# Performance work log

Hardware: AMD Instinct MI355X
Metric: run time of the kernel (lower is better)

The kernel has to match this reference:

```python
import jax, jax.numpy as jnp
import numpy as np

B, T, I, H, O = 64, 512, 128, 1024, 128
ALPHA = 0.2


def setup_inputs() -> dict:
    key = jax.random.key(0)
    ks = jax.random.split(key, 7)
    inv_sqrt_h = 1.0 / np.sqrt(H)
    return {
        "x": jax.random.normal(ks[0], (B, T, I), dtype=jnp.float32),
        "wi": jax.random.normal(ks[1], (I, H), dtype=jnp.float32) / np.sqrt(I),
        "wrec": jax.random.normal(ks[2], (H, H), dtype=jnp.float32) * inv_sqrt_h,
        "wout": jax.random.normal(ks[3], (H, O), dtype=jnp.float32) * inv_sqrt_h,
        "b": jax.random.normal(ks[4], (H, 1), dtype=jnp.float32) * 0.1,
        "g": jax.random.normal(ks[5], (H, 1), dtype=jnp.float32) * 0.5 + 1.0,
        "h0": jax.random.normal(ks[6], (H,), dtype=jnp.float32) * 0.1,
    }


def reference(x, wi, wrec, wout, b, g, h0):
    # Leaky tanh RNN: h_{t+1} = h_t + alpha*(-h_t + (g*r_t) @ wrec^T + x_t @ wi)
    #                 r_t = tanh(h_t + b); out_t = (g*r_t) @ wout
    gv = g[:, 0]  # (H,)
    bv = b[:, 0]  # (H,)
    batch = x.shape[0]

    r0 = jnp.tanh(h0 + bv)                     # (H,)
    out0 = (gv * r0) @ wout                    # (O,) broadcast over batch

    h_init = jnp.broadcast_to(h0, (batch, h0.shape[0]))
    r_init = jnp.broadcast_to(r0, (batch, h0.shape[0]))

    # precompute input projection for all steps used in the loop (steps 0..T-2)
    xs = jnp.swapaxes(x[:, :-1, :], 0, 1)      # (T-1, B, I)

    def step(carry, x_t):
        h, r = carry
        h = h + ALPHA * (-h + (gv * r) @ wrec.T + x_t @ wi)
        r = jnp.tanh(h + bv)
        out = (gv * r) @ wout                  # (B, O)
        return (h, r), out

    _, outs = jax.lax.scan(step, (h_init, r_init), xs)   # (T-1, B, O)
    outs = jnp.swapaxes(outs, 0, 1)                      # (B, T-1, O)
    out0b = jnp.broadcast_to(out0, (batch, 1, wout.shape[1]))
    return jnp.concatenate([out0b, outs], axis=1)        # (B, T, O)
```

## Files before the change

### kernel.cpp

```cpp
#include <hip/hip_runtime.h>

#define H 1024
#define I_DIM 128
#define O_DIM 128
#define T_DIM 512
#define ALPHA 0.2f
#define NWG 64
#define GSZ 16

typedef short short8 __attribute__((ext_vector_type(8)));
typedef float f32x4 __attribute__((ext_vector_type(4)));
typedef unsigned long long ull_alias __attribute__((may_alias));

__device__ __forceinline__ unsigned short f2b(float f) {
    union { float f; unsigned u; } x; x.f = f;
    unsigned u = x.u;
    return (unsigned short)((u + 0x7FFFu + ((u >> 16) & 1u)) >> 16);
}
__device__ __forceinline__ float tanh_fast(float x) {
    float e = __expf(2.0f * x);
    return 1.0f - 2.0f * __builtin_amdgcn_rcpf(e + 1.0f);
}
__device__ __forceinline__ short8 ld8f(const float* __restrict__ p) {
    const float4 a = *(const float4*)p;
    const float4 b = *(const float4*)(p + 4);
    short8 r;
    r[0]=(short)f2b(a.x); r[1]=(short)f2b(a.y); r[2]=(short)f2b(a.z); r[3]=(short)f2b(a.w);
    r[4]=(short)f2b(b.x); r[5]=(short)f2b(b.y); r[6]=(short)f2b(b.z); r[7]=(short)f2b(b.w);
    return r;
}

__global__ __launch_bounds__(256, 1) void rnn_kernel(
    const float* __restrict__ x, const float* __restrict__ wi,
    const float* __restrict__ wrec, const float* __restrict__ wout,
    const float* __restrict__ bb, const float* __restrict__ gg,
    const float* __restrict__ h0p, float* __restrict__ out,
    unsigned short* __restrict__ aG, unsigned int* __restrict__ tagG)
{
    __shared__ unsigned short abuf[32 * 512];
    __shared__ unsigned short aloc[1024];
    __shared__ float opart[4 * 128];

    const int tid  = threadIdx.x;
    const int w    = tid >> 6, lane = tid & 63;
    const int n    = lane & 15, q = lane >> 4;
    const int grp  = blockIdx.x & 3;
    const int ji   = blockIdx.x >> 2;
    const int j0   = ji * 64;
    const int j    = j0 + w * 16 + n;
    const int b0   = grp * 16;
    unsigned int* tg = tagG + grp * 128;

    short8 wfr[32];
#pragma unroll
    for (int kt = 0; kt < 32; ++kt)
        wfr[kt] = ld8f(&wrec[(size_t)j * H + kt * 32 + q * 8]);

    short8 wifr[4];
#pragma unroll
    for (int kt = 0; kt < 4; ++kt) {
        short8 v;
#pragma unroll
        for (int i = 0; i < 8; ++i)
            v[i] = (short)f2b(wi[(size_t)(kt * 32 + q * 8 + i) * H + j]);
        wifr[kt] = v;
    }
    short8 wofr[8];
#pragma unroll
    for (int kk = 0; kk < 8; ++kk) {
        short8 v;
        const int kb = (w * 8 + kk) * 32 + q * 8;
#pragma unroll
        for (int i = 0; i < 8; ++i)
            v[i] = (n < 8) ? (short)f2b(wout[(size_t)(kb + i) * O_DIM + ji * 8 + n]) : (short)0;
        wofr[kk] = v;
    }

    const float gv = gg[j], bv = bb[j], h00 = h0p[j];
    float hreg[4];
#pragma unroll
    for (int r = 0; r < 4; ++r) hreg[r] = h00;

    const int kl    = w * 16 + n;
    const int off_l = (kl >> 5) * 512 + ((kl & 31) >> 3) * 128 + (kl & 7);
    const int slot  = ji * 4 + w;

    auto publish = [&](int t) {
        asm volatile("" ::: "memory");
        unsigned long long v = *(const ull_alias*)&aloc[w * 256 + lane * 4];
        unsigned long long* dst = (unsigned long long*)
            (aG + (size_t)((t & 1) * 4 + grp) * 16384 + ji * 1024 + w * 256 + lane * 4);
        __hip_atomic_store(dst, v, __ATOMIC_RELAXED, __HIP_MEMORY_SCOPE_AGENT);
        asm volatile("s_waitcnt vmcnt(0)" ::: "memory");
        if (lane == 0)
            __hip_atomic_store(&tg[(t & 1) * 64 + slot], (unsigned)t,
                               __ATOMIC_RELAXED, __HIP_MEMORY_SCOPE_AGENT);
    };

    auto consume = [&](int tv) {
        const ull_alias* s64 = (const ull_alias*)
            (aG + (size_t)((tv & 1) * 4 + grp) * 16384) + (size_t)w * 1024;
        unsigned long long vals[16];
#pragma unroll
        for (int i = 0; i < 16; ++i)
            vals[i] = __hip_atomic_load((const unsigned long long*)&s64[i * 64 + lane],
                                        __ATOMIC_RELAXED, __HIP_MEMORY_SCOPE_AGENT);
        asm volatile("" ::: "memory");
        ull_alias* d64 = (ull_alias*)abuf + (size_t)w * 1024;
#pragma unroll
        for (int i = 0; i < 16; ++i)
            d64[i * 64 + lane] = vals[i];
    };

    auto do_out = [&](int t) {
        f32x4 oa = {0.f, 0.f, 0.f, 0.f};
#pragma unroll
        for (int kk = 0; kk < 8; ++kk) {
            short8 af = *(const short8*)&abuf[(w * 8 + kk) * 512 + lane * 8];
            oa = __builtin_amdgcn_mfma_f32_16x16x32_bf16(af, wofr[kk], oa, 0, 0, 0);
        }
        if (n < 8) {
#pragma unroll
            for (int r = 0; r < 4; ++r) opart[w * 128 + (4 * q + r) * 8 + n] = oa[r];
        }
        __syncthreads();
        if (tid < 128) {
            float s = opart[tid] + opart[128 + tid] + opart[256 + tid] + opart[384 + tid];
            const int m = tid >> 3, c = tid & 7;
            out[((size_t)(b0 + m) * T_DIM + t) * O_DIM + ji * 8 + c] = s;
        }
    };

    auto wait_tags = [&](int tv) {
        const unsigned int* tp = tg + (tv & 1) * 64;
        for (;;) {
            unsigned v = __hip_atomic_load(&tp[lane], __ATOMIC_RELAXED,
                                           __HIP_MEMORY_SCOPE_AGENT);
            if (__all(v == (unsigned)tv)) break;
            __builtin_amdgcn_s_sleep(1);
        }
        asm volatile("" ::: "memory");
    };

    {
        unsigned short a0 = f2b(gv * tanh_fast(h00 + bv));
#pragma unroll
        for (int r = 0; r < 4; ++r) aloc[off_l + (4 * q + r) * 8] = a0;
        publish(0);
    }

    short8 xfr[4];
#pragma unroll
    for (int kt = 0; kt < 4; ++kt)
        xfr[kt] = ld8f(&x[(size_t)(b0 + n) * T_DIM * I_DIM + kt * 32 + q * 8]);

    for (int t = 1; t < T_DIM; ++t) {
        f32x4 acc0 = {0.f,0.f,0.f,0.f}, acc1 = {0.f,0.f,0.f,0.f};
        acc0 = __builtin_amdgcn_mfma_f32_16x16x32_bf16(xfr[0], wifr[0], acc0, 0,0,0);
        acc1 = __builtin_amdgcn_mfma_f32_16x16x32_bf16(xfr[1], wifr[1], acc1, 0,0,0);
        acc0 = __builtin_amdgcn_mfma_f32_16x16x32_bf16(xfr[2], wifr[2], acc0, 0,0,0);
        acc1 = __builtin_amdgcn_mfma_f32_16x16x32_bf16(xfr[3], wifr[3], acc1, 0,0,0);

        __syncthreads();
        wait_tags(t - 1);
        consume(t - 1);
        __syncthreads();

#pragma unroll
        for (int kt = 0; kt < 32; kt += 2) {
            short8 a0f = *(const short8*)&abuf[kt * 512 + lane * 8];
            short8 a1f = *(const short8*)&abuf[(kt + 1) * 512 + lane * 8];
            acc0 = __builtin_amdgcn_mfma_f32_16x16x32_bf16(a0f, wfr[kt],     acc0, 0,0,0);
            acc1 = __builtin_amdgcn_mfma_f32_16x16x32_bf16(a1f, wfr[kt + 1], acc1, 0,0,0);
        }

#pragma unroll
        for (int r = 0; r < 4; ++r) {
            float z  = acc0[r] + acc1[r];
            float hv = (1.0f - ALPHA) * hreg[r] + ALPHA * z;
            hreg[r] = hv;
            aloc[off_l + (4 * q + r) * 8] = f2b(gv * tanh_fast(hv + bv));
        }
        publish(t);

        if (t < T_DIM - 1) {
#pragma unroll
            for (int kt = 0; kt < 4; ++kt)
                xfr[kt] = ld8f(&x[((size_t)(b0 + n) * T_DIM + t) * I_DIM + kt * 32 + q * 8]);
        }
        do_out(t - 1);
    }

    __syncthreads();
    wait_tags(T_DIM - 1);
    consume(T_DIM - 1);
    __syncthreads();
    do_out(T_DIM - 1);
}

extern "C" void kernel_launch(void* const* d_in, const int* in_sizes, int n_in,
                              void* d_out, int out_size, void* d_ws, size_t ws_size,
                              hipStream_t stream) {
    const float* x    = (const float*)d_in[0];
    const float* wi   = (const float*)d_in[1];
    const float* wrec = (const float*)d_in[2];
    const float* wout = (const float*)d_in[3];
    const float* bb   = (const float*)d_in[4];
    const float* gg   = (const float*)d_in[5];
    const float* h0   = (const float*)d_in[6];
    float* outp = (float*)d_out;

    unsigned short* aG = (unsigned short*)d_ws;
    unsigned int* tagG = (unsigned int*)((char*)d_ws + 2 * 4 * 16384 * 2);

    hipMemsetAsync(tagG, 0xFF, 4 * 2 * 64 * sizeof(unsigned int), stream);
    hipLaunchKernelGGL(rnn_kernel, dim3(NWG), dim3(256), 0, stream,
                       x, wi, wrec, wout, bb, gg, h0, outp, aG, tagG);
}
```

Before: 1.961 ms.

## Embed step tags in published activation words to drop separate flag handshake

Each 64-bit published word now carries 48 bits of bf16 activation data plus a 16-bit step tag, so consumers poll the data itself instead of waiting on a separate tag array. This removes the vmcnt wait and separate tag store on the producer side and the extra tag-polling round trip on the consumer side, shortening the per-step cross-workgroup latency. The cost is extra pack/unpack bit manipulation and about 1.5x more global traffic per step. Correctness depends on 64-bit atomic stores being seen whole, and the tag repeats only after 65536 steps.

```diff
diff --git a/kernel.cpp b/kernel.cpp
--- a/kernel.cpp
+++ b/kernel.cpp
@@ -7,6 +7,8 @@
 #define ALPHA 0.2f
 #define NWG 64
 #define GSZ 16
+#define SLICE_U64 96
+#define GRP_U64   (64 * SLICE_U64)
 
 typedef short short8 __attribute__((ext_vector_type(8)));
 typedef float f32x4 __attribute__((ext_vector_type(4)));
@@ -35,7 +37,7 @@
     const float* __restrict__ wrec, const float* __restrict__ wout,
     const float* __restrict__ bb, const float* __restrict__ gg,
     const float* __restrict__ h0p, float* __restrict__ out,
-    unsigned short* __restrict__ aG, unsigned int* __restrict__ tagG)
+    unsigned long long* __restrict__ aG)
 {
     __shared__ unsigned short abuf[32 * 512];
     __shared__ unsigned short aloc[1024];
@@ -49,7 +51,6 @@
     const int j0   = ji * 64;
     const int j    = j0 + w * 16 + n;
     const int b0   = grp * 16;
-    unsigned int* tg = tagG + grp * 128;
 
     short8 wfr[32];
 #pragma unroll
@@ -85,31 +86,73 @@
     const int off_l = (kl >> 5) * 512 + ((kl & 31) >> 3) * 128 + (kl & 7);
     const int slot  = ji * 4 + w;
 
+    const int c1 = lane,      os1 = c1 / 3, p1 = c1 - os1 * 3;
+    const int c2 = lane + 64, os2 = c2 / 3, p2 = c2 - os2 * 3;
+    unsigned long long* const pub0 = aG + grp * GRP_U64 + slot * SLICE_U64;
+    unsigned long long* const pub1 = pub0 + 4 * GRP_U64;
+    const unsigned long long* const con0 = aG + grp * GRP_U64;
+    const unsigned long long* const con1 = con0 + 4 * GRP_U64;
+
+    int coff[8];
+#pragma unroll
+    for (int i = 0; i < 8; ++i) {
+        const int kt  = w * 8 + i;
+        const int sub = lane >> 4;
+        const int pw  = (kt & 1) * 2 + (sub >> 1);
+        const int so  = sub & 1;
+        const int m   = lane & 15;
+        coff[i] = ((kt >> 1) * 4 + pw) * SLICE_U64 + (m * 2 + so) * 3;
+    }
+
+    auto pack_chunk = [&](int os, int p) -> unsigned long long {
+        const ull_alias* op = (const ull_alias*)&aloc[w * 256 + (os & 1) * 128 + (os >> 1) * 8];
+        const unsigned long long lo = op[0], hi = op[1];
+        unsigned long long d;
+        if (p == 0)      d = lo & 0x0000FFFFFFFFFFFFull;
+        else if (p == 1) d = ((lo >> 48) | (hi << 16)) & 0x0000FFFFFFFFFFFFull;
+        else             d = ((hi >> 32) | ((hi >> 48) << 32)) & 0x0000FFFFFFFFFFFFull;
+        return d;
+    };
+
     auto publish = [&](int t) {
         asm volatile("" ::: "memory");
-        unsigned long long v = *(const ull_alias*)&aloc[w * 256 + lane * 4];
-        unsigned long long* dst = (unsigned long long*)
-            (aG + (size_t)((t & 1) * 4 + grp) * 16384 + ji * 1024 + w * 256 + lane * 4);
-        __hip_atomic_store(dst, v, __ATOMIC_RELAXED, __HIP_MEMORY_SCOPE_AGENT);
-        asm volatile("s_waitcnt vmcnt(0)" ::: "memory");
-        if (lane == 0)
-            __hip_atomic_store(&tg[(t & 1) * 64 + slot], (unsigned)t,
+        const unsigned long long tagv = (unsigned long long)(unsigned)t << 48;
+        unsigned long long* dst = (t & 1) ? pub1 : pub0;
+        __hip_atomic_store(&dst[c1], pack_chunk(os1, p1) | tagv,
+                           __ATOMIC_RELAXED, __HIP_MEMORY_SCOPE_AGENT);
+        if (lane < 32)
+            __hip_atomic_store(&dst[c2], pack_chunk(os2, p2) | tagv,
                                __ATOMIC_RELAXED, __HIP_MEMORY_SCOPE_AGENT);
     };
 
     auto consume = [&](int tv) {
-        const ull_alias* s64 = (const ull_alias*)
-            (aG + (size_t)((tv & 1) * 4 + grp) * 16384) + (size_t)w * 1024;
-        unsigned long long vals[16];
-#pragma unroll
-        for (int i = 0; i < 16; ++i)
-            vals[i] = __hip_atomic_load((const unsigned long long*)&s64[i * 64 + lane],
-                                        __ATOMIC_RELAXED, __HIP_MEMORY_SCOPE_AGENT);
+        const unsigned tt = (unsigned)tv;
+        const unsigned long long* gb = (tv & 1) ? con1 : con0;
+        unsigned long long v[24];
+        for (;;) {
+#pragma unroll
+            for (int i = 0; i < 8; ++i) {
+                const unsigned long long* cp = gb + coff[i];
+                v[3*i  ] = __hip_atomic_load(cp,     __ATOMIC_RELAXED, __HIP_MEMORY_SCOPE_AGENT);
+                v[3*i+1] = __hip_atomic_load(cp + 1, __ATOMIC_RELAXED, __HIP_MEMORY_SCOPE_AGENT);
+                v[3*i+2] = __hip_atomic_load(cp + 2, __ATOMIC_RELAXED, __HIP_MEMORY_SCOPE_AGENT);
+            }
+            unsigned bad = 0;
+#pragma unroll
+            for (int c = 0; c < 24; ++c) bad |= (unsigned)(v[c] >> 48) ^ tt;
+            if (__all(bad == 0)) break;
+            __builtin_amdgcn_s_sleep(1);
+        }
         asm volatile("" ::: "memory");
-        ull_alias* d64 = (ull_alias*)abuf + (size_t)w * 1024;
-#pragma unroll
-        for (int i = 0; i < 16; ++i)
-            d64[i * 64 + lane] = vals[i];
+#pragma unroll
+        for (int i = 0; i < 8; ++i) {
+            const unsigned long long ca = v[3*i], cb = v[3*i+1], cc = v[3*i+2];
+            const unsigned long long w01 = (ca & 0xFFFFFFFFull)
+                | (((ca >> 32) & 0xFFFFull) << 32) | ((cb & 0xFFFFull) << 48);
+            const unsigned long long w23 = ((cb >> 16) & 0xFFFFFFFFull) | (cc << 32);
+            ull_alias* d = (ull_alias*)((char*)abuf + w * 8192 + (i * 64 + lane) * 16);
+            d[0] = w01; d[1] = w23;
+        }
     };
 
     auto do_out = [&](int t) {
@@ -129,17 +172,6 @@
             const int m = tid >> 3, c = tid & 7;
             out[((size_t)(b0 + m) * T_DIM + t) * O_DIM + ji * 8 + c] = s;
         }
-    };
-
-    auto wait_tags = [&](int tv) {
-        const unsigned int* tp = tg + (tv & 1) * 64;
-        for (;;) {
-            unsigned v = __hip_atomic_load(&tp[lane], __ATOMIC_RELAXED,
-                                           __HIP_MEMORY_SCOPE_AGENT);
-            if (__all(v == (unsigned)tv)) break;
-            __builtin_amdgcn_s_sleep(1);
-        }
-        asm volatile("" ::: "memory");
     };
 
     {
@@ -162,7 +194,6 @@
         acc1 = __builtin_amdgcn_mfma_f32_16x16x32_bf16(xfr[3], wifr[3], acc1, 0,0,0);
 
         __syncthreads();
-        wait_tags(t - 1);
         consume(t - 1);
         __syncthreads();
 
@@ -192,7 +223,6 @@
     }
 
     __syncthreads();
-    wait_tags(T_DIM - 1);
     consume(T_DIM - 1);
     __syncthreads();
     do_out(T_DIM - 1);
@@ -210,10 +240,9 @@
     const float* h0   = (const float*)d_in[6];
     float* outp = (float*)d_out;
 
-    unsigned short* aG = (unsigned short*)d_ws;
-    unsigned int* tagG = (unsigned int*)((char*)d_ws + 2 * 4 * 16384 * 2);
-
-    hipMemsetAsync(tagG, 0xFF, 4 * 2 * 64 * sizeof(unsigned int), stream);
+    unsigned long long* aG = (unsigned long long*)d_ws;
+
+    hipMemsetAsync(d_ws, 0xFF, (size_t)2 * 4 * GRP_U64 * 8, stream);
     hipLaunchKernelGGL(rnn_kernel, dim3(NWG), dim3(256), 0, stream,
-                       x, wi, wrec, wout, bb, gg, h0, outp, aG, tagG);
-}
+                       x, wi, wrec, wout, bb, gg, h0, outp, aG);
+}
```

After: 2.122 ms. 8.2% more time.
